# Kernel tuning notes

Measured on AMD Instinct MI355X. Metric: run time of the kernel, lower is better.

The kernel has to match this reference:

```python
import jax, jax.numpy as jnp
import numpy as np

CHANNELS = 1024
T_LEN = 16384
WINDOW = 16
W_MIN, W_MAX = -1.0, 3.0
BETA = 0.95       # snn.Leaky(beta=0.95)
THRESHOLD = 1.0   # snn.Leaky(threshold=1)


def setup_inputs() -> dict:
    key = jax.random.key(0)
    inp = jax.random.normal(key, (CHANNELS, T_LEN), dtype=jnp.float32)
    return {"inp": inp}


def reference(inp):
    C, T = inp.shape
    pad = WINDOW // 2
    inp_padded = jnp.pad(inp, ((0, 0), (pad, pad)))  # [C, T + WINDOW]
    n_steps = T - WINDOW

    def step(carry, t):
        w, mem = carry
        # B: sliding window [C, WINDOW] starting at column t of padded input
        B = jax.lax.dynamic_slice(inp_padded, (0, t), (C, WINDOW))
        # mean(B @ B.T, axis=1) == B @ mean(B, axis=0)  -- avoids [C, C] intermediate
        B_ram = B @ jnp.mean(B, axis=0)
        w = jnp.clip(0.5 * w + 0.5 * B_ram, W_MIN, W_MAX)
        x = B[:, 0]  # == inp_padded[:, t]
        # snntorch Leaky, reset_mechanism='subtract':
        # reset from incoming mem, then mem = beta*mem + input - reset*thr, spk = mem > thr
        reset = (mem > THRESHOLD).astype(inp.dtype)
        mem = BETA * mem + w * x - reset * THRESHOLD
        spk = (mem > THRESHOLD).astype(inp.dtype)
        return (w, mem), spk

    w0 = jnp.ones((C,), dtype=inp.dtype)
    mem0 = jnp.zeros((C,), dtype=inp.dtype)
    _, spks = jax.lax.scan(step, (w0, mem0), jnp.arange(n_steps))  # spks: [n_steps, C]
    # out = deepcopy(inp); out[:, t] = spk for t < T - WINDOW
    out = inp.at[:, :n_steps].set(spks.T)
    return out
```

## Files before the change

kernel.cpp:

```cpp
#include <hip/hip_runtime.h>

#define C_CH   1024
#define T_DIM  16384
#define NSTEPS (T_DIM - 16)
#define PAD    8
#define TP     (T_DIM + 16)
#define CHUNK  512
#define NCHUNK 32
#define WARM   256

#define WS_CM_OFFSET (8u * T_DIM * sizeof(double))

__global__ void colsum_partial(const float* __restrict__ inp, double* __restrict__ part) {
    int col = blockIdx.x * 256 + threadIdx.x;
    int rc  = blockIdx.y;
    const float* p = inp + (size_t)rc * 128 * T_DIM + col;
    double acc = 0.0;
    #pragma unroll 4
    for (int r = 0; r < 128; ++r) acc += (double)p[(size_t)r * T_DIM];
    part[(size_t)rc * T_DIM + col] = acc;
}

__global__ void colmean_reduce(const double* __restrict__ part, float* __restrict__ cm) {
    int s = blockIdx.x * 256 + threadIdx.x;
    if (s >= TP) return;
    float v = 0.0f;
    if (s >= PAD && s < T_DIM + PAD) {
        int col = s - PAD;
        double t = 0.0;
        #pragma unroll
        for (int r = 0; r < 8; ++r) t += part[(size_t)r * T_DIM + col];
        v = (float)(t * (1.0 / 1024.0));
    }
    cm[s] = v;
}

__global__ __launch_bounds__(64) void scan_kernel(const float* __restrict__ inp,
                                                  const float* __restrict__ cm,
                                                  float* __restrict__ out) {
    const int k  = blockIdx.x;
    const int c  = blockIdx.y * 64 + threadIdx.x;
    const int t0 = k * CHUNK;
    const int tend = min(t0 + CHUNK, NSTEPS);
    const int tw = (k == 0) ? 0 : t0 - WARM;

    const float* row  = inp + (size_t)c * T_DIM;
    float*       orow = out + (size_t)c * T_DIM;

    float xs[16], ms[16];
    double win = 0.0;
    #pragma unroll
    for (int j = 0; j < 16; ++j) {
        int s = tw + j;
        float x = (s >= PAD) ? row[s - PAD] : 0.0f;
        float m = cm[s];
        xs[j] = x; ms[j] = m;
        win += (double)(x * m);
    }

    float w = 1.0f, mem = 0.0f;

    for (int t = tw; t < tend; t += 16) {
        float4 a0 = *(const float4*)(row + t + 8);
        float4 a1 = *(const float4*)(row + t + 12);
        float4 a2 = *(const float4*)(row + t + 16);
        float4 a3 = *(const float4*)(row + t + 20);
        float4 b0 = *(const float4*)(cm + t + 16);
        float4 b1 = *(const float4*)(cm + t + 20);
        float4 b2 = *(const float4*)(cm + t + 24);
        float4 b3 = *(const float4*)(cm + t + 28);
        float xn[16] = {a0.x,a0.y,a0.z,a0.w, a1.x,a1.y,a1.z,a1.w,
                        a2.x,a2.y,a2.z,a2.w, a3.x,a3.y,a3.z,a3.w};
        float mn[16] = {b0.x,b0.y,b0.z,b0.w, b1.x,b1.y,b1.z,b1.w,
                        b2.x,b2.y,b2.z,b2.w, b3.x,b3.y,b3.z,b3.w};
        float spk[16];

        #pragma unroll
        for (int j = 0; j < 16; ++j) {
            float B = (float)win;
            w = fminf(fmaxf(fmaf(0.5f, w, 0.5f * B), -1.0f), 3.0f);
            float x = xs[j];
            float r = (mem > 1.0f) ? 1.0f : 0.0f;
            mem = fmaf(0.95f, mem, fmaf(w, x, -r));
            spk[j] = (mem > 1.0f) ? 1.0f : 0.0f;
            win += (double)(xn[j] * mn[j]) - (double)(x * ms[j]);
            xs[j] = xn[j]; ms[j] = mn[j];
        }

        if (t >= t0) {
            *(float4*)(orow + t)      = make_float4(spk[0],  spk[1],  spk[2],  spk[3]);
            *(float4*)(orow + t + 4)  = make_float4(spk[4],  spk[5],  spk[6],  spk[7]);
            *(float4*)(orow + t + 8)  = make_float4(spk[8],  spk[9],  spk[10], spk[11]);
            *(float4*)(orow + t + 12) = make_float4(spk[12], spk[13], spk[14], spk[15]);
        }
    }
}

__global__ void tail_copy(const float* __restrict__ inp, float* __restrict__ out) {
    int i = blockIdx.x * 256 + threadIdx.x;
    int c = i >> 4, j = i & 15;
    size_t idx = (size_t)c * T_DIM + NSTEPS + j;
    out[idx] = inp[idx];
}

extern "C" void kernel_launch(void* const* d_in, const int* in_sizes, int n_in,
                              void* d_out, int out_size, void* d_ws, size_t ws_size,
                              hipStream_t stream) {
    const float* inp = (const float*)d_in[0];
    float* out = (float*)d_out;
    double* part = (double*)d_ws;
    float* cm = (float*)((char*)d_ws + WS_CM_OFFSET);

    colsum_partial<<<dim3(T_DIM / 256, 8), 256, 0, stream>>>(inp, part);
    colmean_reduce<<<dim3((TP + 255) / 256), 256, 0, stream>>>(part, cm);
    scan_kernel<<<dim3(NCHUNK, C_CH / 64), 64, 0, stream>>>(inp, cm, out);
    tail_copy<<<dim3(64), 256, 0, stream>>>(inp, out);
}
```

Baseline: 167.2 us.

## Halve scan chunks, use float window sum, prefetch loads, fuse tail copy

New measurement: 154.8 us. -7.4%, faster.

```diff
diff --git a/kernel.cpp b/kernel.cpp
--- a/kernel.cpp
+++ b/kernel.cpp
@@ -5,34 +5,45 @@
 #define NSTEPS (T_DIM - 16)
 #define PAD    8
 #define TP     (T_DIM + 16)
-#define CHUNK  512
-#define NCHUNK 32
+#define CHUNK  256
+#define NCHUNK 64
 #define WARM   256
 
 #define WS_CM_OFFSET (8u * T_DIM * sizeof(double))
 
 __global__ void colsum_partial(const float* __restrict__ inp, double* __restrict__ part) {
-    int col = blockIdx.x * 256 + threadIdx.x;
-    int rc  = blockIdx.y;
-    const float* p = inp + (size_t)rc * 128 * T_DIM + col;
-    double acc = 0.0;
+    int col4 = (blockIdx.x * 256 + threadIdx.x) * 4;
+    int rc   = blockIdx.y;
+    const float* p = inp + (size_t)rc * 128 * T_DIM + col4;
+    double ax = 0.0, ay = 0.0, az = 0.0, aw = 0.0;
     #pragma unroll 4
-    for (int r = 0; r < 128; ++r) acc += (double)p[(size_t)r * T_DIM];
-    part[(size_t)rc * T_DIM + col] = acc;
+    for (int r = 0; r < 128; ++r) {
+        float4 v = *(const float4*)(p + (size_t)r * T_DIM);
+        ax += (double)v.x; ay += (double)v.y; az += (double)v.z; aw += (double)v.w;
+    }
+    double* q = part + (size_t)rc * T_DIM + col4;
+    q[0] = ax; q[1] = ay; q[2] = az; q[3] = aw;
 }
 
-__global__ void colmean_reduce(const double* __restrict__ part, float* __restrict__ cm) {
-    int s = blockIdx.x * 256 + threadIdx.x;
-    if (s >= TP) return;
-    float v = 0.0f;
-    if (s >= PAD && s < T_DIM + PAD) {
-        int col = s - PAD;
-        double t = 0.0;
-        #pragma unroll
-        for (int r = 0; r < 8; ++r) t += part[(size_t)r * T_DIM + col];
-        v = (float)(t * (1.0 / 1024.0));
+__global__ void colmean_tail(const double* __restrict__ part, const float* __restrict__ inp,
+                             float* __restrict__ cm, float* __restrict__ out) {
+    int i = blockIdx.x * 256 + threadIdx.x;
+    if (i < TP) {
+        float v = 0.0f;
+        if (i >= PAD && i < T_DIM + PAD) {
+            int col = i - PAD;
+            double t = 0.0;
+            #pragma unroll
+            for (int r = 0; r < 8; ++r) t += part[(size_t)r * T_DIM + col];
+            v = (float)(t * (1.0 / 1024.0));
+        }
+        cm[i] = v;
     }
-    cm[s] = v;
+    if (i < C_CH * 16) {
+        int c = i >> 4, j = i & 15;
+        size_t idx = (size_t)c * T_DIM + NSTEPS + j;
+        out[idx] = inp[idx];
+    }
 }
 
 __global__ __launch_bounds__(64) void scan_kernel(const float* __restrict__ inp,
@@ -48,42 +59,52 @@
     float*       orow = out + (size_t)c * T_DIM;
 
     float xs[16], ms[16];
-    double win = 0.0;
+    float win = 0.0f;
     #pragma unroll
     for (int j = 0; j < 16; ++j) {
         int s = tw + j;
         float x = (s >= PAD) ? row[s - PAD] : 0.0f;
         float m = cm[s];
         xs[j] = x; ms[j] = m;
-        win += (double)(x * m);
+        win = fmaf(x, m, win);
     }
 
     float w = 1.0f, mem = 0.0f;
 
+    float4 a0 = *(const float4*)(row + tw + 8);
+    float4 a1 = *(const float4*)(row + tw + 12);
+    float4 a2 = *(const float4*)(row + tw + 16);
+    float4 a3 = *(const float4*)(row + tw + 20);
+    float4 b0 = *(const float4*)(cm + tw + 16);
+    float4 b1 = *(const float4*)(cm + tw + 20);
+    float4 b2 = *(const float4*)(cm + tw + 24);
+    float4 b3 = *(const float4*)(cm + tw + 28);
+
     for (int t = tw; t < tend; t += 16) {
-        float4 a0 = *(const float4*)(row + t + 8);
-        float4 a1 = *(const float4*)(row + t + 12);
-        float4 a2 = *(const float4*)(row + t + 16);
-        float4 a3 = *(const float4*)(row + t + 20);
-        float4 b0 = *(const float4*)(cm + t + 16);
-        float4 b1 = *(const float4*)(cm + t + 20);
-        float4 b2 = *(const float4*)(cm + t + 24);
-        float4 b3 = *(const float4*)(cm + t + 28);
         float xn[16] = {a0.x,a0.y,a0.z,a0.w, a1.x,a1.y,a1.z,a1.w,
                         a2.x,a2.y,a2.z,a2.w, a3.x,a3.y,a3.z,a3.w};
         float mn[16] = {b0.x,b0.y,b0.z,b0.w, b1.x,b1.y,b1.z,b1.w,
                         b2.x,b2.y,b2.z,b2.w, b3.x,b3.y,b3.z,b3.w};
+
+        int ts = (t + 16 < tend) ? (t + 16) : t;
+        a0 = *(const float4*)(row + ts + 8);
+        a1 = *(const float4*)(row + ts + 12);
+        a2 = *(const float4*)(row + ts + 16);
+        a3 = *(const float4*)(row + ts + 20);
+        b0 = *(const float4*)(cm + ts + 16);
+        b1 = *(const float4*)(cm + ts + 20);
+        b2 = *(const float4*)(cm + ts + 24);
+        b3 = *(const float4*)(cm + ts + 28);
+
         float spk[16];
-
         #pragma unroll
         for (int j = 0; j < 16; ++j) {
-            float B = (float)win;
-            w = fminf(fmaxf(fmaf(0.5f, w, 0.5f * B), -1.0f), 3.0f);
+            w = fminf(fmaxf(fmaf(0.5f, w, 0.5f * win), -1.0f), 3.0f);
             float x = xs[j];
             float r = (mem > 1.0f) ? 1.0f : 0.0f;
             mem = fmaf(0.95f, mem, fmaf(w, x, -r));
             spk[j] = (mem > 1.0f) ? 1.0f : 0.0f;
-            win += (double)(xn[j] * mn[j]) - (double)(x * ms[j]);
+            win = fmaf(xn[j], mn[j], fmaf(-x, ms[j], win));
             xs[j] = xn[j]; ms[j] = mn[j];
         }
 
@@ -96,13 +117,6 @@
     }
 }
 
-__global__ void tail_copy(const float* __restrict__ inp, float* __restrict__ out) {
-    int i = blockIdx.x * 256 + threadIdx.x;
-    int c = i >> 4, j = i & 15;
-    size_t idx = (size_t)c * T_DIM + NSTEPS + j;
-    out[idx] = inp[idx];
-}
-
 extern "C" void kernel_launch(void* const* d_in, const int* in_sizes, int n_in,
                               void* d_out, int out_size, void* d_ws, size_t ws_size,
                               hipStream_t stream) {
@@ -111,8 +125,7 @@
     double* part = (double*)d_ws;
     float* cm = (float*)((char*)d_ws + WS_CM_OFFSET);
 
-    colsum_partial<<<dim3(T_DIM / 256, 8), 256, 0, stream>>>(inp, part);
-    colmean_reduce<<<dim3((TP + 255) / 256), 256, 0, stream>>>(part, cm);
+    colsum_partial<<<dim3(T_DIM / 1024, 8), 256, 0, stream>>>(inp, part);
+    colmean_tail<<<dim3(65), 256, 0, stream>>>(part, inp, cm, out);
     scan_kernel<<<dim3(NCHUNK, C_CH / 64), 64, 0, stream>>>(inp, cm, out);
-    tail_copy<<<dim3(64), 256, 0, stream>>>(inp, out);
 }
```
